# Optimization experiments

Hardware: AMD Instinct MI355X
Metric: run time of the kernel (lower is better)

The kernel has to match this reference:

```python
import jax, jax.numpy as jnp
import numpy as np

N = 32768
E = 524288
NFEAT = 256
NHID = 256
NUM_HEADS = 4
HEAD_DIM = NHID // NUM_HEADS
NLAYER = 2
EPS = 1e-5


def setup_inputs():
    keys = iter(jax.random.split(jax.random.key(0), 64))

    def nrm(shape, scale=0.05):
        return jax.random.normal(next(keys), shape, dtype=jnp.float32) * scale

    inp = {
        "x": jax.random.normal(next(keys), (N, NFEAT), dtype=jnp.float32),
        "edge_src": jax.random.randint(next(keys), (E,), 0, N),
        "edge_dst": jax.random.randint(next(keys), (E,), 0, N),
        "edge_attr": jax.random.uniform(next(keys), (E,), dtype=jnp.float32) * 0.1,
        "num_graphs": 64,
    }
    for i in range(NLAYER):
        fin = NFEAT if i == 0 else NHID
        inp["conv_w%d" % i] = nrm((fin, NHID))
        inp["bn_g%d" % i] = jnp.ones((NHID,), jnp.float32)
        inp["bn_b%d" % i] = jnp.zeros((NHID,), jnp.float32)
        inp["bn_m%d" % i] = nrm((NHID,), 0.1)
        inp["bn_v%d" % i] = 1.0 + jax.random.uniform(next(keys), (NHID,), dtype=jnp.float32) * 0.1
        inp["attn_in_w%d" % i] = nrm((3 * NHID, NHID))
        inp["attn_in_b%d" % i] = jnp.zeros((3 * NHID,), jnp.float32)
        inp["attn_out_w%d" % i] = nrm((NHID, NHID))
        inp["attn_out_b%d" % i] = jnp.zeros((NHID,), jnp.float32)
        inp["ln_g%d" % i] = jnp.ones((NHID,), jnp.float32)
        inp["ln_b%d" % i] = jnp.zeros((NHID,), jnp.float32)
    inp["score_w"] = nrm((1, NHID))
    inp["score_b"] = jnp.zeros((1,), jnp.float32)
    return inp


def _mha(xb, iw, ib, ow, ob):
    # torch.nn.MultiheadAttention (batch_first), all graphs same length so
    # key_padding_mask is all-False (no masked positions).
    B, S, H = xb.shape
    q, k, v = jnp.split(xb @ iw.T + ib, 3, axis=-1)
    heads = lambda t: t.reshape(B, S, NUM_HEADS, HEAD_DIM).transpose(0, 2, 1, 3)
    q, k, v = heads(q), heads(k), heads(v)
    scale = jnp.float32(1.0 / np.sqrt(HEAD_DIM))
    att = jax.nn.softmax(jnp.einsum("bhqd,bhkd->bhqk", q, k) * scale, axis=-1)
    o = jnp.einsum("bhqk,bhkd->bhqd", att, v).transpose(0, 2, 1, 3).reshape(B, S, H)
    return o @ ow.T + ob


def _forward(x, edge_attr, params, edge_src, edge_dst, num_graphs):
    n = x.shape[0]
    B = num_graphs
    S = n // B  # equal-sized graphs -> max_nodes == S, pad is a no-op
    h = x
    for i, (cw, bng, bnb, bnm, bnv, iw, ib, ow, ob, lg, lb) in enumerate(params):
        # DIGCNConv: out[dst] += edge_attr * (x @ W)[src]
        conv = jax.ops.segment_sum(edge_attr[:, None] * (h @ cw)[edge_src], edge_dst, num_segments=n)
        # BatchNorm1d (eval mode, running stats)
        conv = (conv - bnm) * jax.lax.rsqrt(bnv + EPS) * bng + bnb
        # ragged gather -> pad/stack -> MHA -> unpad (equal graph sizes => reshape)
        attended = _mha(conv.reshape(B, S, NHID), iw, ib, ow, ob).reshape(n, NHID)
        y = conv + attended
        mu = jnp.mean(y, axis=-1, keepdims=True)
        var = jnp.mean((y - mu) ** 2, axis=-1, keepdims=True)
        h = (y - mu) * jax.lax.rsqrt(var + EPS) * lg + lb  # LayerNorm
        if i < NLAYER - 1:
            h = jax.nn.relu(h)
    return h


def reference(x, edge_src, edge_dst, edge_attr, num_graphs,
              conv_w0, bn_g0, bn_b0, bn_m0, bn_v0, attn_in_w0, attn_in_b0, attn_out_w0, attn_out_b0, ln_g0, ln_b0,
              conv_w1, bn_g1, bn_b1, bn_m1, bn_v1, attn_in_w1, attn_in_b1, attn_out_w1, attn_out_b1, ln_g1, ln_b1,
              score_w, score_b):
    params = [
        (conv_w0, bn_g0, bn_b0, bn_m0, bn_v0, attn_in_w0, attn_in_b0, attn_out_w0, attn_out_b0, ln_g0, ln_b0),
        (conv_w1, bn_g1, bn_b1, bn_m1, bn_v1, attn_in_w1, attn_in_b1, attn_out_w1, attn_out_b1, ln_g1, ln_b1),
    ]
    h = _forward(x, edge_attr, params, edge_src, edge_dst, num_graphs)
    scores = (h @ score_w.T + score_b)[:, 0]
    # emb_list / score_list are per-graph views of these flat arrays
    return h, scores
```

## Files before the change

kernel.cpp:

```cpp
#include <hip/hip_runtime.h>
#include <hip/hip_bf16.h>
#include <math.h>

#define N_NODES 32768
#define E_EDGES 524288
#define NHID    256
#define HEAD_DIM 64
#define SEQ     512
#define EPS_LN  1e-5f
#define SM_SCALE 0.18033688011112042f

typedef __hip_bfloat16 bf16;
typedef __attribute__((ext_vector_type(8))) short short8;
typedef __attribute__((ext_vector_type(4))) float floatx4;
static const size_t NH = (size_t)N_NODES * NHID;

__device__ __forceinline__ void unpack2(unsigned int u, float& lo, float& hi) {
    union { float f; unsigned int i; } a, b;
    a.i = u << 16; b.i = u & 0xffff0000u;
    lo = a.f; hi = b.f;
}

__device__ __forceinline__ void* swzp(void* base, int row, int col) {
    return (char*)base + (((row << 7) + (col << 1)) ^ ((row & 7) << 4));
}

__device__ __forceinline__ void gload16(const bf16* g, void* lds) {
    __builtin_amdgcn_global_load_lds((const __attribute__((address_space(1))) void*)g,
                                     (__attribute__((address_space(3))) void*)lds, 16, 0, 0);
}

__global__ void k_cvtb4(bf16* __restrict__ dst, const float* __restrict__ src) {
    size_t i = (size_t)(blockIdx.x * 256 + threadIdx.x) * 4;
    const float4 v = *(const float4*)(src + i);
    __align__(8) bf16 tmp[4];
    tmp[0] = __float2bfloat16(v.x);
    tmp[1] = __float2bfloat16(v.y);
    tmp[2] = __float2bfloat16(v.z);
    tmp[3] = __float2bfloat16(v.w);
    *(uint2*)(dst + i) = *(uint2*)tmp;
}

__global__ __launch_bounds__(256) void k_stage(const float* __restrict__ cw,
                                               const float* __restrict__ bng,
                                               const float* __restrict__ bnb,
                                               const float* __restrict__ bnm,
                                               const float* __restrict__ bnv,
                                               const float* __restrict__ iw,
                                               const float* __restrict__ ow,
                                               bf16* __restrict__ iwb,
                                               bf16* __restrict__ owb,
                                               bf16* __restrict__ cwT,
                                               float* __restrict__ bns,
                                               float* __restrict__ bnt) {
    const int blk = blockIdx.x;
    const int tid = threadIdx.x;
    if (blk < 256) {
        const float* src = (blk < 192) ? iw : ow;
        bf16* dst = (blk < 192) ? iwb : owb;
        size_t i = (size_t)((blk < 192 ? blk : blk - 192) * 256 + tid) * 4;
        const float4 v = *(const float4*)(src + i);
        __align__(8) bf16 t4[4];
        t4[0] = __float2bfloat16(v.x);
        t4[1] = __float2bfloat16(v.y);
        t4[2] = __float2bfloat16(v.z);
        t4[3] = __float2bfloat16(v.w);
        *(uint2*)(dst + i) = *(uint2*)t4;
    } else if (blk < 512) {
        const int k = blk - 256;
        cwT[(size_t)tid * 256 + k] = __float2bfloat16(cw[(size_t)k * 256 + tid]);
    } else {
        float sv = bng[tid] * rsqrtf(bnv[tid] + EPS_LN);
        bns[tid] = sv;
        bnt[tid] = bnb[tid] - bnm[tid] * sv;
    }
}

__global__ void k_hist(const int* __restrict__ edst, int* __restrict__ counts) {
    int e = blockIdx.x * 256 + threadIdx.x;
    atomicAdd(&counts[edst[e]], 1);
}

__global__ __launch_bounds__(256) void k_scan(const int* __restrict__ counts,
                                              int* __restrict__ offsets,
                                              int* __restrict__ cursor) {
    __shared__ int sums[256];
    const int tid = threadIdx.x;
    const int base = tid * 128;
    int s = 0;
    for (int i = 0; i < 128; ++i) s += counts[base + i];
    sums[tid] = s;
    __syncthreads();
    for (int off = 1; off < 256; off <<= 1) {
        int v = (tid >= off) ? sums[tid - off] : 0;
        __syncthreads();
        sums[tid] += v;
        __syncthreads();
    }
    int run = (tid == 0) ? 0 : sums[tid - 1];
    for (int i = 0; i < 128; ++i) {
        int c = counts[base + i];
        offsets[base + i] = run;
        cursor[base + i] = run;
        run += c;
    }
    if (tid == 255) offsets[32768] = run;
}

__global__ void k_fill(const int* __restrict__ esrc, const int* __restrict__ edst,
                       const float* __restrict__ eattr, int* __restrict__ cursor,
                       int* __restrict__ srcp, float* __restrict__ attrp) {
    int e = blockIdx.x * 256 + threadIdx.x;
    int d = edst[e];
    int slot = atomicAdd(&cursor[d], 1);
    srcp[slot] = esrc[e];
    attrp[slot] = eattr[e];
}

__global__ __launch_bounds__(256) void k_gather(const bf16* __restrict__ t,
                                                const int* __restrict__ offsets,
                                                const int* __restrict__ srcp,
                                                const float* __restrict__ attrp,
                                                const float* __restrict__ bns,
                                                const float* __restrict__ bnt,
                                                bf16* __restrict__ conv) {
    const int node = (blockIdx.x * 256 + threadIdx.x) >> 6;
    const int lane = threadIdx.x & 63;
    const int half = lane >> 5;
    const int l32 = lane & 31;
    const int start = offsets[node];
    const int end = offsets[node + 1];
    float a[8];
#pragma unroll
    for (int i = 0; i < 8; ++i) a[i] = 0.f;
    for (int c0 = start; c0 < end; c0 += 64) {
        const int n = min(64, end - c0);
        int sidx = 0;
        float sa = 0.f;
        if (lane < n) {
            sidx = srcp[c0 + lane];
            sa = attrp[c0 + lane];
        }
        for (int j = 0; j < n; j += 2) {
            const int e = j + half;
            const int s = __shfl(sidx, e, 64);
            const float aw = __shfl(sa, e, 64);
            const uint4 u = *(const uint4*)(t + (size_t)s * 256 + l32 * 8);
            float v0, v1, v2, v3, v4, v5, v6, v7;
            unpack2(u.x, v0, v1);
            unpack2(u.y, v2, v3);
            unpack2(u.z, v4, v5);
            unpack2(u.w, v6, v7);
            a[0] = fmaf(aw, v0, a[0]);
            a[1] = fmaf(aw, v1, a[1]);
            a[2] = fmaf(aw, v2, a[2]);
            a[3] = fmaf(aw, v3, a[3]);
            a[4] = fmaf(aw, v4, a[4]);
            a[5] = fmaf(aw, v5, a[5]);
            a[6] = fmaf(aw, v6, a[6]);
            a[7] = fmaf(aw, v7, a[7]);
        }
    }
#pragma unroll
    for (int i = 0; i < 8; ++i) a[i] += __shfl_xor(a[i], 32, 64);
    if (half == 0) {
        const int c = l32 * 8;
        const float4 s0 = *(const float4*)(bns + c);
        const float4 s1 = *(const float4*)(bns + c + 4);
        const float4 t0 = *(const float4*)(bnt + c);
        const float4 t1 = *(const float4*)(bnt + c + 4);
        __align__(16) bf16 tmp[8];
        tmp[0] = __float2bfloat16(fmaf(a[0], s0.x, t0.x));
        tmp[1] = __float2bfloat16(fmaf(a[1], s0.y, t0.y));
        tmp[2] = __float2bfloat16(fmaf(a[2], s0.z, t0.z));
        tmp[3] = __float2bfloat16(fmaf(a[3], s0.w, t0.w));
        tmp[4] = __float2bfloat16(fmaf(a[4], s1.x, t1.x));
        tmp[5] = __float2bfloat16(fmaf(a[5], s1.y, t1.y));
        tmp[6] = __float2bfloat16(fmaf(a[6], s1.z, t1.z));
        tmp[7] = __float2bfloat16(fmaf(a[7], s1.w, t1.w));
        *(uint4*)(conv + (size_t)node * 256 + c) = *(uint4*)tmp;
    }
}

__global__ __launch_bounds__(256) void k_gemm(const bf16* __restrict__ A,
                                              const bf16* __restrict__ WT,
                                              const float* __restrict__ bias,
                                              bf16* __restrict__ C, bf16* __restrict__ VT,
                                              int ldc, int qkvmode) {
    __shared__ __align__(16) short As[128 * 64];
    __shared__ __align__(16) short Bs[128 * 64];
    const int tid = threadIdx.x;
    const int bm = blockIdx.x * 128;
    const int bn = blockIdx.y * 128;
    const int wid = tid >> 6;
    const int lane = tid & 63;
    const int wr = (wid >> 1) * 64;
    const int wc = (wid & 1) * 64;
    const int quad = lane >> 4;
    const int l16 = lane & 15;

    floatx4 acc[4][4];
#pragma unroll
    for (int mi = 0; mi < 4; ++mi)
#pragma unroll
        for (int ni = 0; ni < 4; ++ni)
            acc[mi][ni] = (floatx4){0.f, 0.f, 0.f, 0.f};

    for (int k0 = 0; k0 < 256; k0 += 64) {
#pragma unroll
        for (int t = 0; t < 4; ++t) {
            const int p = ((t * 4 + wid) << 10) + (lane << 4);
            const int row = p >> 7;
            const int cb = (p & 127) ^ ((row & 7) << 4);
            gload16(A + (size_t)(bm + row) * 256 + k0 + (cb >> 1),
                    (char*)As + ((t * 4 + wid) << 10));
            gload16(WT + (size_t)(bn + row) * 256 + k0 + (cb >> 1),
                    (char*)Bs + ((t * 4 + wid) << 10));
        }
        __syncthreads();
#pragma unroll
        for (int kk = 0; kk < 2; ++kk) {
            const int kcol = kk * 32 + quad * 8;
            short8 af[4], bfr[4];
#pragma unroll
            for (int mi = 0; mi < 4; ++mi)
                af[mi] = *(const short8*)swzp(As, wr + mi * 16 + l16, kcol);
#pragma unroll
            for (int ni = 0; ni < 4; ++ni)
                bfr[ni] = *(const short8*)swzp(Bs, wc + ni * 16 + l16, kcol);
#pragma unroll
            for (int mi = 0; mi < 4; ++mi)
#pragma unroll
                for (int ni = 0; ni < 4; ++ni)
                    acc[mi][ni] = __builtin_amdgcn_mfma_f32_16x16x32_bf16(af[mi], bfr[ni],
                                                                          acc[mi][ni], 0, 0, 0);
        }
        __syncthreads();
    }
    const float cs = (qkvmode && bn < 256) ? SM_SCALE : 1.0f;
    const bool vpath = (qkvmode && bn >= 512);
#pragma unroll
    for (int ni = 0; ni < 4; ++ni) {
        const int gc = bn + wc + ni * 16 + l16;
        const float bv = bias ? bias[gc] : 0.f;
#pragma unroll
        for (int mi = 0; mi < 4; ++mi) {
            const int gr = bm + wr + mi * 16 + quad * 4;
            if (vpath) {
                const int head = (gc - 512) >> 6;
                const int d = (gc - 512) & 63;
                const int bg = gr >> 9;
                const int sl = gr & 511;
                __align__(8) bf16 t4[4];
#pragma unroll
                for (int r = 0; r < 4; ++r) t4[r] = __float2bfloat16(acc[mi][ni][r] + bv);
                *(uint2*)(VT + (((size_t)((bg * 4 + head) * 64 + d)) << 9) + sl) = *(uint2*)t4;
            } else {
#pragma unroll
                for (int r = 0; r < 4; ++r)
                    C[(size_t)(gr + r) * ldc + gc] = __float2bfloat16((acc[mi][ni][r] + bv) * cs);
            }
        }
    }
}

__global__ __launch_bounds__(256) void k_fattn(const bf16* __restrict__ qkv,
                                               const bf16* __restrict__ vtb,
                                               bf16* __restrict__ ctx) {
    const int bid = ((blockIdx.x & 7) << 8) | (blockIdx.x >> 3);
    const int qt = bid & 7;
    const int head = (bid >> 3) & 3;
    const int b = bid >> 5;
    const int tid = threadIdx.x;
    const int wave = tid >> 6;
    const int lane = tid & 63;
    const int quad = lane >> 4;
    const int l16 = lane & 15;
    const int qrow0 = b * SEQ + qt * 64 + wave * 16;

    __shared__ __align__(16) short Ks[2][64 * 64];
    __shared__ __align__(16) short Vt[2][64 * 64];
    __shared__ __align__(16) short Ps[4][16 * 64];

    const bf16* kbase = qkv + (size_t)(b * SEQ) * 768 + 256 + head * HEAD_DIM;
    const bf16* vbase = vtb + (size_t)((b * 4 + head) * 64) * 512;
    const int pbase = (wave << 10) + (lane << 4);

    short8 af_q[2];
    {
        const bf16* qp = qkv + (size_t)(qrow0 + l16) * 768 + head * HEAD_DIM + quad * 8;
        af_q[0] = *(const short8*)(qp);
        af_q[1] = *(const short8*)(qp + 32);
    }
    short8 ones;
#pragma unroll
    for (int j = 0; j < 8; ++j) ones[j] = (short)0x3F80;

    floatx4 acc[5];
#pragma unroll
    for (int nt = 0; nt < 5; ++nt) acc[nt] = (floatx4){0.f, 0.f, 0.f, 0.f};

    auto STAGE = [&](int kt2, int bf) {
#pragma unroll
        for (int i = 0; i < 2; ++i) {
            const int p = (i << 12) + pbase;
            const int row = p >> 7;
            const int cb = (p & 127) ^ ((row & 7) << 4);
            gload16(kbase + (size_t)(kt2 * 64 + row) * 768 + (cb >> 1),
                    (char*)Ks[bf] + (i << 12) + (wave << 10));
            gload16(vbase + (size_t)row * 512 + kt2 * 64 + (cb >> 1),
                    (char*)Vt[bf] + (i << 12) + (wave << 10));
        }
    };

    STAGE(0, 0);
    __syncthreads();

    for (int kt = 0; kt < 8; ++kt) {
        const int buf = kt & 1;
        if (kt < 7) STAGE(kt + 1, buf ^ 1);

        floatx4 sf[4];
        __builtin_amdgcn_s_setprio(1);
#pragma unroll
        for (int f = 0; f < 4; ++f) {
            const short8 bk0 = *(const short8*)swzp(Ks[buf], f * 16 + l16, quad * 8);
            const short8 bk1 = *(const short8*)swzp(Ks[buf], f * 16 + l16, 32 + quad * 8);
            sf[f] = __builtin_amdgcn_mfma_f32_16x16x32_bf16(af_q[0], bk0,
                                                            (floatx4){0.f, 0.f, 0.f, 0.f}, 0, 0, 0);
            sf[f] = __builtin_amdgcn_mfma_f32_16x16x32_bf16(af_q[1], bk1, sf[f], 0, 0, 0);
        }
        __builtin_amdgcn_s_setprio(0);

        bf16* psb = (bf16*)&Ps[wave][0];
#pragma unroll
        for (int r = 0; r < 4; ++r) {
            const float p0 = exp2f(fminf(sf[0][r], 80.f));
            const float p1 = exp2f(fminf(sf[1][r], 80.f));
            const float p2 = exp2f(fminf(sf[2][r], 80.f));
            const float p3 = exp2f(fminf(sf[3][r], 80.f));
            const int qr = quad * 4 + r;
            *(bf16*)swzp(psb, qr, l16)      = __float2bfloat16(p0);
            *(bf16*)swzp(psb, qr, 16 + l16) = __float2bfloat16(p1);
            *(bf16*)swzp(psb, qr, 32 + l16) = __float2bfloat16(p2);
            *(bf16*)swzp(psb, qr, 48 + l16) = __float2bfloat16(p3);
        }

        __builtin_amdgcn_s_setprio(1);
#pragma unroll
        for (int c2 = 0; c2 < 2; ++c2) {
            const short8 ap = *(const short8*)swzp(psb, l16, c2 * 32 + quad * 8);
#pragma unroll
            for (int nt = 0; nt < 4; ++nt) {
                const short8 bv = *(const short8*)swzp(Vt[buf], nt * 16 + l16, c2 * 32 + quad * 8);
                acc[nt] = __builtin_amdgcn_mfma_f32_16x16x32_bf16(ap, bv, acc[nt], 0, 0, 0);
            }
            acc[4] = __builtin_amdgcn_mfma_f32_16x16x32_bf16(ap, ones, acc[4], 0, 0, 0);
        }
        __builtin_amdgcn_s_setprio(0);
        __syncthreads();
    }

#pragma unroll
    for (int r = 0; r < 4; ++r) {
        const float inv = 1.f / acc[4][r];
        bf16* op = ctx + (size_t)(qrow0 + quad * 4 + r) * 256 + head * HEAD_DIM + l16;
        op[0]  = __float2bfloat16(acc[0][r] * inv);
        op[16] = __float2bfloat16(acc[1][r] * inv);
        op[32] = __float2bfloat16(acc[2][r] * inv);
        op[48] = __float2bfloat16(acc[3][r] * inv);
    }
}

__global__ void k_ln(const bf16* __restrict__ conv, const bf16* __restrict__ proj,
                     const float* __restrict__ lg, const float* __restrict__ lb,
                     bf16* __restrict__ h) {
    int gt = blockIdx.x * blockDim.x + threadIdx.x;
    int node = gt >> 6;
    int lane = gt & 63;
    size_t base = (size_t)node * 256 + lane * 4;
    uint2 ua = *(const uint2*)(conv + base);
    uint2 up = *(const uint2*)(proj + base);
    float a0, a1, a2, a3, p0, p1, p2, p3;
    unpack2(ua.x, a0, a1);
    unpack2(ua.y, a2, a3);
    unpack2(up.x, p0, p1);
    unpack2(up.y, p2, p3);
    float y0 = a0 + p0, y1 = a1 + p1, y2 = a2 + p2, y3 = a3 + p3;
    float sum = y0 + y1 + y2 + y3;
#pragma unroll
    for (int off = 32; off > 0; off >>= 1) sum += __shfl_xor(sum, off, 64);
    float mu = sum * (1.0f / 256.0f);
    float d0 = y0 - mu, d1 = y1 - mu, d2 = y2 - mu, d3 = y3 - mu;
    float vs = d0 * d0 + d1 * d1 + d2 * d2 + d3 * d3;
#pragma unroll
    for (int off = 32; off > 0; off >>= 1) vs += __shfl_xor(vs, off, 64);
    float r = rsqrtf(vs * (1.0f / 256.0f) + EPS_LN);
    int c = lane * 4;
    float o0 = fmaxf(fmaf(d0 * r, lg[c + 0], lb[c + 0]), 0.f);
    float o1 = fmaxf(fmaf(d1 * r, lg[c + 1], lb[c + 1]), 0.f);
    float o2 = fmaxf(fmaf(d2 * r, lg[c + 2], lb[c + 2]), 0.f);
    float o3 = fmaxf(fmaf(d3 * r, lg[c + 3], lb[c + 3]), 0.f);
    __align__(8) bf16 tmp[4];
    tmp[0] = __float2bfloat16(o0);
    tmp[1] = __float2bfloat16(o1);
    tmp[2] = __float2bfloat16(o2);
    tmp[3] = __float2bfloat16(o3);
    *(uint2*)(h + base) = *(uint2*)tmp;
}

__global__ void k_lnout(const bf16* __restrict__ conv, const bf16* __restrict__ proj,
                        const float* __restrict__ lg, const float* __restrict__ lb,
                        const float* __restrict__ sw, const float* __restrict__ sb,
                        float* __restrict__ out) {
    int gt = blockIdx.x * blockDim.x + threadIdx.x;
    int node = gt >> 6;
    int lane = gt & 63;
    size_t base = (size_t)node * 256 + lane * 4;
    uint2 ua = *(const uint2*)(conv + base);
    uint2 up = *(const uint2*)(proj + base);
    float a0, a1, a2, a3, p0, p1, p2, p3;
    unpack2(ua.x, a0, a1);
    unpack2(ua.y, a2, a3);
    unpack2(up.x, p0, p1);
    unpack2(up.y, p2, p3);
    float y0 = a0 + p0, y1 = a1 + p1, y2 = a2 + p2, y3 = a3 + p3;
    float sum = y0 + y1 + y2 + y3;
#pragma unroll
    for (int off = 32; off > 0; off >>= 1) sum += __shfl_xor(sum, off, 64);
    float mu = sum * (1.0f / 256.0f);
    float d0 = y0 - mu, d1 = y1 - mu, d2 = y2 - mu, d3 = y3 - mu;
    float vs = d0 * d0 + d1 * d1 + d2 * d2 + d3 * d3;
#pragma unroll
    for (int off = 32; off > 0; off >>= 1) vs += __shfl_xor(vs, off, 64);
    float r = rsqrtf(vs * (1.0f / 256.0f) + EPS_LN);
    int c = lane * 4;
    float o0 = fmaf(d0 * r, lg[c + 0], lb[c + 0]);
    float o1 = fmaf(d1 * r, lg[c + 1], lb[c + 1]);
    float o2 = fmaf(d2 * r, lg[c + 2], lb[c + 2]);
    float o3 = fmaf(d3 * r, lg[c + 3], lb[c + 3]);
    *(float4*)(out + base) = make_float4(o0, o1, o2, o3);
    float part = o0 * sw[c + 0] + o1 * sw[c + 1] + o2 * sw[c + 2] + o3 * sw[c + 3];
#pragma unroll
    for (int off = 32; off > 0; off >>= 1) part += __shfl_xor(part, off, 64);
    if (lane == 0)
        out[(size_t)N_NODES * 256 + node] = part + sb[0];
}

extern "C" void kernel_launch(void* const* d_in, const int* in_sizes, int n_in,
                              void* d_out, int out_size, void* d_ws, size_t ws_size,
                              hipStream_t stream) {
    if (ws_size < (size_t)100663296) return;

    const float* x     = (const float*)d_in[0];
    const int*   esrc  = (const int*)d_in[1];
    const int*   edst  = (const int*)d_in[2];
    const float* eattr = (const float*)d_in[3];

    bf16* convb = (bf16*)d_ws;
    bf16* qkvb  = convb + NH;
    bf16* tb    = qkvb + 3 * NH;
    bf16* vtb   = tb + NH;
    bf16* xb  = qkvb;
    bf16* hb  = qkvb + NH;
    bf16* pjb = qkvb;

    char* scr = (char*)d_out;
    const size_t LBYTES = 393216 + 131072 + 131072 + 2048;
    int*   counts  = (int*)(scr + 2 * LBYTES);
    int*   offsets = counts + 32768;
    int*   cursor  = offsets + 32769;
    int*   srcp    = cursor + 32768;
    float* attrp   = (float*)(srcp + E_EDGES);

    (void)hipMemsetAsync(counts, 0, 32768 * sizeof(int), stream);
    k_hist<<<E_EDGES / 256, 256, 0, stream>>>(edst, counts);
    k_scan<<<1, 256, 0, stream>>>(counts, offsets, cursor);
    k_fill<<<E_EDGES / 256, 256, 0, stream>>>(esrc, edst, eattr, cursor, srcp, attrp);

    for (int L = 0; L < 2; ++L) {
        int bi = 5 + L * 11;
        char* base = scr + (size_t)L * LBYTES;
        bf16*  iwb = (bf16*)base;
        bf16*  owb = iwb + 196608;
        bf16*  cwT = owb + 65536;
        float* bns = (float*)(cwT + 65536);
        float* bnt = bns + 256;
        k_stage<<<513, 256, 0, stream>>>((const float*)d_in[bi + 0], (const float*)d_in[bi + 1],
                                         (const float*)d_in[bi + 2], (const float*)d_in[bi + 3],
                                         (const float*)d_in[bi + 4], (const float*)d_in[bi + 5],
                                         (const float*)d_in[bi + 7], iwb, owb, cwT, bns, bnt);
    }

    k_cvtb4<<<8192, 256, 0, stream>>>(xb, x);

    for (int L = 0; L < 2; ++L) {
        int bi = 5 + L * 11;
        char* base = scr + (size_t)L * LBYTES;
        bf16*  iwb = (bf16*)base;
        bf16*  owb = iwb + 196608;
        bf16*  cwT = owb + 65536;
        float* bns = (float*)(cwT + 65536);
        float* bnt = bns + 256;
        const float* ib = (const float*)d_in[bi + 6];
        const float* ob = (const float*)d_in[bi + 8];

        k_gemm<<<dim3(256, 2), 256, 0, stream>>>(L == 0 ? xb : hb, cwT, nullptr, tb, nullptr,
                                                 256, 0);
        k_gather<<<8192, 256, 0, stream>>>(tb, offsets, srcp, attrp, bns, bnt, convb);
        k_gemm<<<dim3(256, 6), 256, 0, stream>>>(convb, iwb, ib, qkvb, vtb, 768, 1);
        k_fattn<<<2048, 256, 0, stream>>>(qkvb, vtb, tb);
        k_gemm<<<dim3(256, 2), 256, 0, stream>>>(tb, owb, ob, pjb, nullptr, 256, 0);
        if (L == 0) {
            k_ln<<<8192, 256, 0, stream>>>(convb, pjb, (const float*)d_in[bi + 9],
                                           (const float*)d_in[bi + 10], hb);
        } else {
            k_lnout<<<8192, 256, 0, stream>>>(convb, pjb, (const float*)d_in[bi + 9],
                                              (const float*)d_in[bi + 10],
                                              (const float*)d_in[27], (const float*)d_in[28],
                                              (float*)d_out);
        }
    }
}
```

Before: 523.3 us.

## Double-buffer GEMM LDS tiles and load attention K/V directly from global

The GEMM kernel gains a second shared-memory buffer for the A and B tiles, so the next K-slice is staged while MFMAs run on the current one, hiding global load latency. The attention kernel drops its shared-memory K/V staging, barriers and priority hints, and each wave reads K rows and transposed V fragments straight from global memory, relying on cache for reuse across the four waves. This removes block-level syncs and LDS traffic in attention, but multiplies global/L2 requests and exposes load latency without explicit prefetch. The GEMM doubles LDS use to 64KB per block, which may reduce occupancy.

```diff
diff --git a/kernel.cpp b/kernel.cpp
--- a/kernel.cpp
+++ b/kernel.cpp
@@ -187,8 +187,8 @@
                                               const float* __restrict__ bias,
                                               bf16* __restrict__ C, bf16* __restrict__ VT,
                                               int ldc, int qkvmode) {
-    __shared__ __align__(16) short As[128 * 64];
-    __shared__ __align__(16) short Bs[128 * 64];
+    __shared__ __align__(16) short As[2][128 * 64];
+    __shared__ __align__(16) short Bs[2][128 * 64];
     const int tid = threadIdx.x;
     const int bm = blockIdx.x * 128;
     const int bn = blockIdx.y * 128;
@@ -206,28 +206,34 @@
         for (int ni = 0; ni < 4; ++ni)
             acc[mi][ni] = (floatx4){0.f, 0.f, 0.f, 0.f};
 
-    for (int k0 = 0; k0 < 256; k0 += 64) {
+    auto STAGE = [&](int ks, int bf) {
 #pragma unroll
         for (int t = 0; t < 4; ++t) {
             const int p = ((t * 4 + wid) << 10) + (lane << 4);
             const int row = p >> 7;
             const int cb = (p & 127) ^ ((row & 7) << 4);
-            gload16(A + (size_t)(bm + row) * 256 + k0 + (cb >> 1),
-                    (char*)As + ((t * 4 + wid) << 10));
-            gload16(WT + (size_t)(bn + row) * 256 + k0 + (cb >> 1),
-                    (char*)Bs + ((t * 4 + wid) << 10));
-        }
-        __syncthreads();
+            gload16(A + (size_t)(bm + row) * 256 + ks * 64 + (cb >> 1),
+                    (char*)&As[bf][0] + ((t * 4 + wid) << 10));
+            gload16(WT + (size_t)(bn + row) * 256 + ks * 64 + (cb >> 1),
+                    (char*)&Bs[bf][0] + ((t * 4 + wid) << 10));
+        }
+    };
+
+    STAGE(0, 0);
+    __syncthreads();
+    for (int t = 0; t < 4; ++t) {
+        const int buf = t & 1;
+        if (t < 3) STAGE(t + 1, buf ^ 1);
 #pragma unroll
         for (int kk = 0; kk < 2; ++kk) {
             const int kcol = kk * 32 + quad * 8;
             short8 af[4], bfr[4];
 #pragma unroll
             for (int mi = 0; mi < 4; ++mi)
-                af[mi] = *(const short8*)swzp(As, wr + mi * 16 + l16, kcol);
+                af[mi] = *(const short8*)swzp(&As[buf][0], wr + mi * 16 + l16, kcol);
 #pragma unroll
             for (int ni = 0; ni < 4; ++ni)
-                bfr[ni] = *(const short8*)swzp(Bs, wc + ni * 16 + l16, kcol);
+                bfr[ni] = *(const short8*)swzp(&Bs[buf][0], wc + ni * 16 + l16, kcol);
 #pragma unroll
             for (int mi = 0; mi < 4; ++mi)
 #pragma unroll
@@ -278,13 +284,10 @@
     const int l16 = lane & 15;
     const int qrow0 = b * SEQ + qt * 64 + wave * 16;
 
-    __shared__ __align__(16) short Ks[2][64 * 64];
-    __shared__ __align__(16) short Vt[2][64 * 64];
     __shared__ __align__(16) short Ps[4][16 * 64];
 
-    const bf16* kbase = qkv + (size_t)(b * SEQ) * 768 + 256 + head * HEAD_DIM;
-    const bf16* vbase = vtb + (size_t)((b * 4 + head) * 64) * 512;
-    const int pbase = (wave << 10) + (lane << 4);
+    const bf16* krow = qkv + (size_t)(b * SEQ + l16) * 768 + 256 + head * HEAD_DIM + quad * 8;
+    const bf16* vrow = vtb + (size_t)((b * 4 + head) * 64 + l16) * 512 + quad * 8;
 
     short8 af_q[2];
     {
@@ -300,39 +303,20 @@
 #pragma unroll
     for (int nt = 0; nt < 5; ++nt) acc[nt] = (floatx4){0.f, 0.f, 0.f, 0.f};
 
-    auto STAGE = [&](int kt2, int bf) {
-#pragma unroll
-        for (int i = 0; i < 2; ++i) {
-            const int p = (i << 12) + pbase;
-            const int row = p >> 7;
-            const int cb = (p & 127) ^ ((row & 7) << 4);
-            gload16(kbase + (size_t)(kt2 * 64 + row) * 768 + (cb >> 1),
-                    (char*)Ks[bf] + (i << 12) + (wave << 10));
-            gload16(vbase + (size_t)row * 512 + kt2 * 64 + (cb >> 1),
-                    (char*)Vt[bf] + (i << 12) + (wave << 10));
-        }
-    };
-
-    STAGE(0, 0);
-    __syncthreads();
+    bf16* psb = (bf16*)&Ps[wave][0];
 
     for (int kt = 0; kt < 8; ++kt) {
-        const int buf = kt & 1;
-        if (kt < 7) STAGE(kt + 1, buf ^ 1);
-
         floatx4 sf[4];
-        __builtin_amdgcn_s_setprio(1);
 #pragma unroll
         for (int f = 0; f < 4; ++f) {
-            const short8 bk0 = *(const short8*)swzp(Ks[buf], f * 16 + l16, quad * 8);
-            const short8 bk1 = *(const short8*)swzp(Ks[buf], f * 16 + l16, 32 + quad * 8);
+            const bf16* kp = krow + (size_t)(kt * 64 + f * 16) * 768;
+            const short8 bk0 = *(const short8*)(kp);
+            const short8 bk1 = *(const short8*)(kp + 32);
             sf[f] = __builtin_amdgcn_mfma_f32_16x16x32_bf16(af_q[0], bk0,
                                                             (floatx4){0.f, 0.f, 0.f, 0.f}, 0, 0, 0);
             sf[f] = __builtin_amdgcn_mfma_f32_16x16x32_bf16(af_q[1], bk1, sf[f], 0, 0, 0);
         }
-        __builtin_amdgcn_s_setprio(0);
-
-        bf16* psb = (bf16*)&Ps[wave][0];
+
 #pragma unroll
         for (int r = 0; r < 4; ++r) {
             const float p0 = exp2f(fminf(sf[0][r], 80.f));
@@ -346,19 +330,17 @@
             *(bf16*)swzp(psb, qr, 48 + l16) = __float2bfloat16(p3);
         }
 
-        __builtin_amdgcn_s_setprio(1);
 #pragma unroll
         for (int c2 = 0; c2 < 2; ++c2) {
             const short8 ap = *(const short8*)swzp(psb, l16, c2 * 32 + quad * 8);
 #pragma unroll
             for (int nt = 0; nt < 4; ++nt) {
-                const short8 bv = *(const short8*)swzp(Vt[buf], nt * 16 + l16, c2 * 32 + quad * 8);
+                const short8 bv =
+                    *(const short8*)(vrow + (size_t)(nt * 16) * 512 + kt * 64 + c2 * 32);
                 acc[nt] = __builtin_amdgcn_mfma_f32_16x16x32_bf16(ap, bv, acc[nt], 0, 0, 0);
             }
             acc[4] = __builtin_amdgcn_mfma_f32_16x16x32_bf16(ap, ones, acc[4], 0, 0, 0);
         }
-        __builtin_amdgcn_s_setprio(0);
-        __syncthreads();
     }
 
 #pragma unroll
```

New measurement: 663.9 us. 26.9% more time.
